# Optimization experiments

Hardware: AMD Instinct MI355X
Metric: run time of the kernel (lower is better)

## Reference

```python
import jax, jax.numpy as jnp
import numpy as np

D = 768      # qkv.in_features (ViT-Base)
R = 16       # LoRA rank
T = 8        # task_id: number of previously saved adapters
B_, S_ = 32, 256
TAU = 1.0


def setup_inputs() -> dict:
    key = jax.random.key(0)
    ks = jax.random.split(key, 13)
    s = lambda k, shape, sc=0.02: jax.random.normal(k, shape, jnp.float32) * sc
    return {
        "x": jax.random.normal(ks[0], (B_, S_, D), jnp.float32),
        "qkv_w": s(ks[1], (3 * D, D)),           # torch Linear weight [out,in]
        "qkv_b": s(ks[2], (3 * D,)),
        "la_q": s(ks[3], (R, D)),                # current-task LoRA A_q [r,d]
        "lb_q": s(ks[4], (D, R)),                # current-task LoRA B_q [d,r]
        "la_v": s(ks[5], (R, D)),
        "lb_v": s(ks[6], (D, R)),
        "A_q": s(ks[7], (T, R, D)),              # saved per-task A_q stacks
        "B_q": s(ks[8], (T, D, R)),
        "A_v": s(ks[9], (T, R, D)),
        "B_v": s(ks[10], (T, D, R)),
        "gate_logits": jax.random.normal(ks[11], (T,), jnp.float32),
        "alpha": jnp.ones((T + 1,), jnp.float32),  # gumbel_gate.alpha, indexed by task_id
    }


def _moe_branch(x, A, B, beta):
    """Weighted sum over T tasks of (x @ A_t^T @ B_t^T) / (||A_t||*||B_t||), weight beta_t.

    Vectorizes the per-task serial low-rank matmuls of the torch loop into two
    batched einsums; beta/norm scaling is folded into B to avoid materializing
    per-task [B,S,D] outputs.
    """
    nA = jnp.sqrt(jnp.sum(A * A, axis=(1, 2)))   # [T] Frobenius norms
    nB = jnp.sqrt(jnp.sum(B * B, axis=(1, 2)))
    scale = beta / (nA * nB)                      # [T]
    za = jnp.einsum('bsd,trd->bstr', x, A)       # [B,S,T,r]
    Bs = B * scale[:, None, None]                 # [T,D,r]
    return jnp.einsum('bstr,tdr->bsd', za, Bs)   # [B,S,D]


def _lora(x, a, b):
    # torch: b(a(x)) with Linear weights a:[r,d], b:[d,r]
    return jnp.einsum('bsr,dr->bsd', jnp.einsum('bsd,rd->bsr', x, a), b)


def reference(x, qkv_w, qkv_b, la_q, lb_q, la_v, lb_v, A_q, B_q, A_v, B_v, gate_logits, alpha):
    # Gumbel-softmax gate over tasks (deterministic/eval path: softmax(logits/tau), hard=False)
    beta = jax.nn.softmax(gate_logits / TAU)
    a_cur = alpha[T]  # alpha[self.task_id]
    new_q = _moe_branch(x, A_q, B_q, beta) + a_cur * _lora(x, la_q, lb_q)
    new_v = _moe_branch(x, A_v, B_v, beta) + a_cur * _lora(x, la_v, lb_v)
    qkv = jnp.einsum('bsd,ed->bse', x, qkv_w) + qkv_b  # [B,S,3D]
    qkv = qkv.at[..., :D].add(new_q)
    qkv = qkv.at[..., 2 * D:].add(new_v)
    return qkv
```

## Files before the change

### kernel.cpp

```cpp
#include <hip/hip_runtime.h>

#define TOK 8192
#define DD  768
#define NOUT 2304
#define TT  8
#define RR  16
#define KRANK 144

typedef __bf16 bf16;
typedef __bf16 bf16x4 __attribute__((ext_vector_type(4)));
typedef __bf16 bf16x8 __attribute__((ext_vector_type(8)));
typedef float  floatx4 __attribute__((ext_vector_type(4)));

__device__ __forceinline__ void gl_lds16(const void* g, void* l) {
    __builtin_amdgcn_global_load_lds((const __attribute__((address_space(1))) void*)g,
                                     (__attribute__((address_space(3))) void*)l, 16, 0, 0);
}

__global__ __launch_bounds__(256) void norms_kernel(
    const float* __restrict__ A_q, const float* __restrict__ B_q,
    const float* __restrict__ A_v, const float* __restrict__ B_v,
    float* __restrict__ norms)
{
    const int b = blockIdx.x;
    const float* base;
    switch (b >> 3) {
        case 0: base = A_q; break;
        case 1: base = B_q; break;
        case 2: base = A_v; break;
        default: base = B_v; break;
    }
    base += (b & 7) * (RR * DD);
    float s = 0.f;
    for (int i = threadIdx.x; i < RR * DD; i += 256) {
        float v = base[i];
        s = fmaf(v, v, s);
    }
    #pragma unroll
    for (int off = 32; off > 0; off >>= 1) s += __shfl_down(s, off);
    __shared__ float ws4[4];
    if ((threadIdx.x & 63) == 0) ws4[threadIdx.x >> 6] = s;
    __syncthreads();
    if (threadIdx.x == 0)
        norms[b] = sqrtf(ws4[0] + ws4[1] + ws4[2] + ws4[3]);
}

__global__ __launch_bounds__(64) void scales_kernel(
    const float* __restrict__ gate_logits, const float* __restrict__ alpha,
    const float* __restrict__ norms, float* __restrict__ scales)
{
    if (threadIdx.x == 0) {
        float mx = gate_logits[0];
        for (int t = 1; t < TT; ++t) mx = fmaxf(mx, gate_logits[t]);
        float e[TT], s = 0.f;
        for (int t = 0; t < TT; ++t) { e[t] = __expf(gate_logits[t] - mx); s += e[t]; }
        for (int t = 0; t < TT; ++t) {
            float beta = e[t] / s;
            scales[t]      = beta / (norms[t]      * norms[8 + t]);
            scales[8 + t]  = beta / (norms[16 + t] * norms[24 + t]);
        }
        scales[16] = alpha[TT];
    }
}

__global__ __launch_bounds__(256) void cast_x_kernel(
    const float* __restrict__ x, bf16* __restrict__ xb)
{
    const int idx = (blockIdx.x * 256 + threadIdx.x) * 4;
    const float4 v = *(const float4*)(x + idx);
    bf16x4 o = { (bf16)v.x, (bf16)v.y, (bf16)v.z, (bf16)v.w };
    *(bf16x4*)(xb + idx) = o;
}

__global__ __launch_bounds__(256) void cast_mid_kernel(
    const float* __restrict__ w, bf16* __restrict__ Wc)
{
    const int idx = DD * DD + (blockIdx.x * 256 + threadIdx.x) * 4;
    const float4 v = *(const float4*)(w + idx);
    bf16x4 o = { (bf16)v.x, (bf16)v.y, (bf16)v.z, (bf16)v.w };
    *(bf16x4*)(Wc + idx) = o;
}

__global__ __launch_bounds__(256) void fold_kernel(
    const float* __restrict__ qkv_w,
    const float* __restrict__ A_q, const float* __restrict__ la_q,
    const float* __restrict__ B_q, const float* __restrict__ lb_q,
    const float* __restrict__ A_v, const float* __restrict__ la_v,
    const float* __restrict__ B_v, const float* __restrict__ lb_v,
    const float* __restrict__ scales, bf16* __restrict__ Wc)
{
    __shared__ float c_lds[8 * KRANK];
    const int tid = threadIdx.x;
    const int d = blockIdx.x * 256 + tid;
    const int gy = blockIdx.y;
    const bool is_v = (gy >= 96);
    const int e0 = (is_v ? gy - 96 : gy) * 8;
    const float* Astack = is_v ? A_v : A_q;
    const float* la     = is_v ? la_v : la_q;
    const float* Bmat   = is_v ? B_v : B_q;
    const float* lb     = is_v ? lb_v : lb_q;
    const float* sc     = scales + (is_v ? 8 : 0);
    const float a_cur   = scales[16];
    const int rowbase   = (is_v ? 2 * DD : 0) + e0;

    for (int idx = tid; idx < 8 * KRANK; idx += 256) {
        const int j = idx / KRANK, i = idx - j * KRANK;
        const int e = e0 + j;
        float v;
        if (i < TT * RR) {
            const int t = i >> 4, r = i & 15;
            v = sc[t] * Bmat[(t * DD + e) * RR + r];
        } else {
            v = a_cur * lb[e * RR + (i - TT * RR)];
        }
        c_lds[j * KRANK + i] = v;
    }
    __syncthreads();

    float acc[8] = {0.f, 0.f, 0.f, 0.f, 0.f, 0.f, 0.f, 0.f};

    for (int i = 0; i < TT * RR; i += 4) {
        const float a0 = Astack[(i + 0) * DD + d];
        const float a1 = Astack[(i + 1) * DD + d];
        const float a2 = Astack[(i + 2) * DD + d];
        const float a3 = Astack[(i + 3) * DD + d];
        #pragma unroll
        for (int j = 0; j < 8; ++j) {
            const float4 cv = *(const float4*)&c_lds[j * KRANK + i];
            acc[j] = fmaf(a0, cv.x, fmaf(a1, cv.y, fmaf(a2, cv.z, fmaf(a3, cv.w, acc[j]))));
        }
    }
    #pragma unroll
    for (int i = 0; i < RR; i += 4) {
        const float a0 = la[(i + 0) * DD + d];
        const float a1 = la[(i + 1) * DD + d];
        const float a2 = la[(i + 2) * DD + d];
        const float a3 = la[(i + 3) * DD + d];
        #pragma unroll
        for (int j = 0; j < 8; ++j) {
            const float4 cv = *(const float4*)&c_lds[j * KRANK + TT * RR + i];
            acc[j] = fmaf(a0, cv.x, fmaf(a1, cv.y, fmaf(a2, cv.z, fmaf(a3, cv.w, acc[j]))));
        }
    }

    #pragma unroll
    for (int j = 0; j < 8; ++j) {
        const int row = rowbase + j;
        Wc[row * DD + d] = (bf16)(qkv_w[row * DD + d] + acc[j]);
    }
}

__global__ __launch_bounds__(256, 2) void gemm_kernel(
    const bf16* __restrict__ A, const bf16* __restrict__ B,
    const float* __restrict__ bias, float* __restrict__ C)
{
    __shared__ bf16 lds_a[128 * 64];
    __shared__ bf16 lds_b[128 * 64];
    const int tid  = threadIdx.x;
    const int lane = tid & 63;
    const int wave = tid >> 6;
    const int m0 = blockIdx.y * 128;
    const int n0 = blockIdx.x * 128;
    const int wm = (wave >> 1) * 64;
    const int wn = (wave & 1) * 64;

    const int srow = lane >> 3;
    const int scol = (lane & 7) * 8;

    floatx4 acc[4][4];
    #pragma unroll
    for (int i = 0; i < 4; ++i)
        #pragma unroll
        for (int j = 0; j < 4; ++j)
            acc[i][j] = (floatx4){0.f, 0.f, 0.f, 0.f};

    for (int kt = 0; kt < DD / 64; ++kt) {
        const int k0 = kt * 64;
        #pragma unroll
        for (int i = 0; i < 4; ++i) {
            const int j = i * 4 + wave;
            const int row = j * 8 + srow;
            gl_lds16(A + (m0 + row) * DD + k0 + scol, &lds_a[j * 512]);
            gl_lds16(B + (n0 + row) * DD + k0 + scol, &lds_b[j * 512]);
        }
        __syncthreads();
        #pragma unroll
        for (int ks = 0; ks < 2; ++ks) {
            bf16x8 af[4], bfr[4];
            const int kofs = ks * 32 + (lane >> 4) * 8;
            #pragma unroll
            for (int mt = 0; mt < 4; ++mt)
                af[mt] = *(const bf16x8*)&lds_a[(wm + mt * 16 + (lane & 15)) * 64 + kofs];
            #pragma unroll
            for (int nt = 0; nt < 4; ++nt)
                bfr[nt] = *(const bf16x8*)&lds_b[(wn + nt * 16 + (lane & 15)) * 64 + kofs];
            #pragma unroll
            for (int mt = 0; mt < 4; ++mt)
                #pragma unroll
                for (int nt = 0; nt < 4; ++nt)
                    acc[mt][nt] = __builtin_amdgcn_mfma_f32_16x16x32_bf16(
                        af[mt], bfr[nt], acc[mt][nt], 0, 0, 0);
        }
        __syncthreads();
    }

    const int cr = (lane >> 4) * 4;
    const int cc = lane & 15;
    #pragma unroll
    for (int nt = 0; nt < 4; ++nt) {
        const int gn = n0 + wn + nt * 16 + cc;
        const float bv = bias[gn];
        #pragma unroll
        for (int mt = 0; mt < 4; ++mt) {
            const int gmb = m0 + wm + mt * 16 + cr;
            #pragma unroll
            for (int r = 0; r < 4; ++r)
                C[(gmb + r) * NOUT + gn] = acc[mt][nt][r] + bv;
        }
    }
}

extern "C" void kernel_launch(void* const* d_in, const int* in_sizes, int n_in,
                              void* d_out, int out_size, void* d_ws, size_t ws_size,
                              hipStream_t stream)
{
    const float* x           = (const float*)d_in[0];
    const float* qkv_w       = (const float*)d_in[1];
    const float* qkv_b       = (const float*)d_in[2];
    const float* la_q        = (const float*)d_in[3];
    const float* lb_q        = (const float*)d_in[4];
    const float* la_v        = (const float*)d_in[5];
    const float* lb_v        = (const float*)d_in[6];
    const float* A_q         = (const float*)d_in[7];
    const float* B_q         = (const float*)d_in[8];
    const float* A_v         = (const float*)d_in[9];
    const float* B_v         = (const float*)d_in[10];
    const float* gate_logits = (const float*)d_in[11];
    const float* alpha       = (const float*)d_in[12];
    float* out = (float*)d_out;

    char* ws = (char*)d_ws;
    bf16*  Xbf    = (bf16*)ws;
    bf16*  Wc     = (bf16*)(ws + 12582912);
    float* norms  = (float*)(ws + 12582912 + 3538944);
    float* scales = norms + 32;

    norms_kernel <<<32, 256, 0, stream>>>(A_q, B_q, A_v, B_v, norms);
    scales_kernel<<<1, 64, 0, stream>>>(gate_logits, alpha, norms, scales);
    cast_x_kernel<<<TOK * DD / 1024, 256, 0, stream>>>(x, Xbf);
    cast_mid_kernel<<<DD * DD / 1024, 256, 0, stream>>>(qkv_w, Wc);
    fold_kernel  <<<dim3(3, 192), 256, 0, stream>>>(qkv_w,
                                                    A_q, la_q, B_q, lb_q,
                                                    A_v, la_v, B_v, lb_v,
                                                    scales, Wc);
    gemm_kernel  <<<dim3(NOUT / 128, TOK / 128), 256, 0, stream>>>(Xbf, Wc, qkv_b, out);
}
```

Before: 195.4 us.

## Merge prep kernels, XOR-swizzle LDS tiles, and remap GEMM blocks across XCDs

Six launches become three. The norm computation and the x bf16 cast now share one prep kernel. The softmax scale computation and the middle-weight cast move into the fold kernel, which each block computes redundantly. The GEMM now applies an XOR swizzle to LDS column chunks to cut bank conflicts on fragment reads, and remaps block indices so that blocks on the same XCD share M tiles for better L2 reuse. The goal is lower launch overhead and faster GEMM inner loops, at the cost of per-block softmax recomputation and mixed-role kernels.

```diff
diff --git a/kernel.cpp b/kernel.cpp
--- a/kernel.cpp
+++ b/kernel.cpp
@@ -17,68 +17,40 @@
                                      (__attribute__((address_space(3))) void*)l, 16, 0, 0);
 }
 
-__global__ __launch_bounds__(256) void norms_kernel(
+__global__ __launch_bounds__(256) void prep_kernel(
     const float* __restrict__ A_q, const float* __restrict__ B_q,
     const float* __restrict__ A_v, const float* __restrict__ B_v,
+    const float* __restrict__ x, bf16* __restrict__ xb,
     float* __restrict__ norms)
 {
+    __shared__ float ws4[4];
     const int b = blockIdx.x;
-    const float* base;
-    switch (b >> 3) {
-        case 0: base = A_q; break;
-        case 1: base = B_q; break;
-        case 2: base = A_v; break;
-        default: base = B_v; break;
-    }
-    base += (b & 7) * (RR * DD);
-    float s = 0.f;
-    for (int i = threadIdx.x; i < RR * DD; i += 256) {
-        float v = base[i];
-        s = fmaf(v, v, s);
-    }
-    #pragma unroll
-    for (int off = 32; off > 0; off >>= 1) s += __shfl_down(s, off);
-    __shared__ float ws4[4];
-    if ((threadIdx.x & 63) == 0) ws4[threadIdx.x >> 6] = s;
-    __syncthreads();
-    if (threadIdx.x == 0)
-        norms[b] = sqrtf(ws4[0] + ws4[1] + ws4[2] + ws4[3]);
-}
-
-__global__ __launch_bounds__(64) void scales_kernel(
-    const float* __restrict__ gate_logits, const float* __restrict__ alpha,
-    const float* __restrict__ norms, float* __restrict__ scales)
-{
-    if (threadIdx.x == 0) {
-        float mx = gate_logits[0];
-        for (int t = 1; t < TT; ++t) mx = fmaxf(mx, gate_logits[t]);
-        float e[TT], s = 0.f;
-        for (int t = 0; t < TT; ++t) { e[t] = __expf(gate_logits[t] - mx); s += e[t]; }
-        for (int t = 0; t < TT; ++t) {
-            float beta = e[t] / s;
-            scales[t]      = beta / (norms[t]      * norms[8 + t]);
-            scales[8 + t]  = beta / (norms[16 + t] * norms[24 + t]);
-        }
-        scales[16] = alpha[TT];
-    }
-}
-
-__global__ __launch_bounds__(256) void cast_x_kernel(
-    const float* __restrict__ x, bf16* __restrict__ xb)
-{
-    const int idx = (blockIdx.x * 256 + threadIdx.x) * 4;
-    const float4 v = *(const float4*)(x + idx);
-    bf16x4 o = { (bf16)v.x, (bf16)v.y, (bf16)v.z, (bf16)v.w };
-    *(bf16x4*)(xb + idx) = o;
-}
-
-__global__ __launch_bounds__(256) void cast_mid_kernel(
-    const float* __restrict__ w, bf16* __restrict__ Wc)
-{
-    const int idx = DD * DD + (blockIdx.x * 256 + threadIdx.x) * 4;
-    const float4 v = *(const float4*)(w + idx);
-    bf16x4 o = { (bf16)v.x, (bf16)v.y, (bf16)v.z, (bf16)v.w };
-    *(bf16x4*)(Wc + idx) = o;
+    if (b < 32) {
+        const float* base;
+        switch (b >> 3) {
+            case 0: base = A_q; break;
+            case 1: base = B_q; break;
+            case 2: base = A_v; break;
+            default: base = B_v; break;
+        }
+        base += (b & 7) * (RR * DD);
+        float s = 0.f;
+        for (int i = threadIdx.x; i < RR * DD; i += 256) {
+            float v = base[i];
+            s = fmaf(v, v, s);
+        }
+        #pragma unroll
+        for (int off = 32; off > 0; off >>= 1) s += __shfl_down(s, off);
+        if ((threadIdx.x & 63) == 0) ws4[threadIdx.x >> 6] = s;
+        __syncthreads();
+        if (threadIdx.x == 0)
+            norms[b] = sqrtf(ws4[0] + ws4[1] + ws4[2] + ws4[3]);
+    } else {
+        const int idx = ((b - 32) * 256 + threadIdx.x) * 4;
+        const float4 v = *(const float4*)(x + idx);
+        bf16x4 o = { (bf16)v.x, (bf16)v.y, (bf16)v.z, (bf16)v.w };
+        *(bf16x4*)(xb + idx) = o;
+    }
 }
 
 __global__ __launch_bounds__(256) void fold_kernel(
@@ -87,21 +59,46 @@
     const float* __restrict__ B_q, const float* __restrict__ lb_q,
     const float* __restrict__ A_v, const float* __restrict__ la_v,
     const float* __restrict__ B_v, const float* __restrict__ lb_v,
-    const float* __restrict__ scales, bf16* __restrict__ Wc)
-{
-    __shared__ float c_lds[8 * KRANK];
+    const float* __restrict__ gate_logits, const float* __restrict__ alpha,
+    const float* __restrict__ norms, bf16* __restrict__ Wc)
+{
     const int tid = threadIdx.x;
     const int d = blockIdx.x * 256 + tid;
     const int gy = blockIdx.y;
-    const bool is_v = (gy >= 96);
-    const int e0 = (is_v ? gy - 96 : gy) * 8;
+
+    if (gy >= 96 && gy < 192) {
+        const int rowbase = DD + (gy - 96) * 8;
+        #pragma unroll
+        for (int j = 0; j < 8; ++j) {
+            const int row = rowbase + j;
+            Wc[row * DD + d] = (bf16)qkv_w[row * DD + d];
+        }
+        return;
+    }
+
+    __shared__ float c_lds[8 * KRANK];
+    __shared__ float sc_sh[TT];
+    __shared__ float acur_sh;
+
+    const bool is_v = (gy >= 192);
+    const int e0 = (is_v ? gy - 192 : gy) * 8;
     const float* Astack = is_v ? A_v : A_q;
     const float* la     = is_v ? la_v : la_q;
     const float* Bmat   = is_v ? B_v : B_q;
     const float* lb     = is_v ? lb_v : lb_q;
-    const float* sc     = scales + (is_v ? 8 : 0);
-    const float a_cur   = scales[16];
+    const float* nA     = norms + (is_v ? 16 : 0);
+    const float* nB     = norms + (is_v ? 24 : 8);
     const int rowbase   = (is_v ? 2 * DD : 0) + e0;
+
+    if (tid == 0) {
+        float mx = gate_logits[0];
+        for (int t = 1; t < TT; ++t) mx = fmaxf(mx, gate_logits[t]);
+        float e[TT], s = 0.f;
+        for (int t = 0; t < TT; ++t) { e[t] = __expf(gate_logits[t] - mx); s += e[t]; }
+        for (int t = 0; t < TT; ++t) sc_sh[t] = (e[t] / s) / (nA[t] * nB[t]);
+        acur_sh = alpha[TT];
+    }
+    __syncthreads();
 
     for (int idx = tid; idx < 8 * KRANK; idx += 256) {
         const int j = idx / KRANK, i = idx - j * KRANK;
@@ -109,9 +106,9 @@
         float v;
         if (i < TT * RR) {
             const int t = i >> 4, r = i & 15;
-            v = sc[t] * Bmat[(t * DD + e) * RR + r];
+            v = sc_sh[t] * Bmat[(t * DD + e) * RR + r];
         } else {
-            v = a_cur * lb[e * RR + (i - TT * RR)];
+            v = acur_sh * lb[e * RR + (i - TT * RR)];
         }
         c_lds[j * KRANK + i] = v;
     }
@@ -159,13 +156,20 @@
     const int tid  = threadIdx.x;
     const int lane = tid & 63;
     const int wave = tid >> 6;
-    const int m0 = blockIdx.y * 128;
-    const int n0 = blockIdx.x * 128;
+
+    const int flat  = blockIdx.y * gridDim.x + blockIdx.x;
+    const int xcd   = flat & 7;
+    const int local = flat >> 3;
+    const int mb    = xcd * 8 + (local & 7);
+    const int nb    = local >> 3;
+    const int m0 = mb * 128;
+    const int n0 = nb * 128;
+
     const int wm = (wave >> 1) * 64;
     const int wn = (wave & 1) * 64;
 
     const int srow = lane >> 3;
-    const int scol = (lane & 7) * 8;
+    const int scol = ((lane & 7) ^ srow) * 8;
 
     floatx4 acc[4][4];
     #pragma unroll
@@ -187,13 +191,17 @@
         #pragma unroll
         for (int ks = 0; ks < 2; ++ks) {
             bf16x8 af[4], bfr[4];
-            const int kofs = ks * 32 + (lane >> 4) * 8;
-            #pragma unroll
-            for (int mt = 0; mt < 4; ++mt)
-                af[mt] = *(const bf16x8*)&lds_a[(wm + mt * 16 + (lane & 15)) * 64 + kofs];
-            #pragma unroll
-            for (int nt = 0; nt < 4; ++nt)
-                bfr[nt] = *(const bf16x8*)&lds_b[(wn + nt * 16 + (lane & 15)) * 64 + kofs];
+            const int c_log = ks * 4 + (lane >> 4);
+            #pragma unroll
+            for (int mt = 0; mt < 4; ++mt) {
+                const int r = wm + mt * 16 + (lane & 15);
+                af[mt] = *(const bf16x8*)&lds_a[r * 64 + ((c_log ^ (r & 7)) * 8)];
+            }
+            #pragma unroll
+            for (int nt = 0; nt < 4; ++nt) {
+                const int r = wn + nt * 16 + (lane & 15);
+                bfr[nt] = *(const bf16x8*)&lds_b[r * 64 + ((c_log ^ (r & 7)) * 8)];
+            }
             #pragma unroll
             for (int mt = 0; mt < 4; ++mt)
                 #pragma unroll
@@ -243,15 +251,12 @@
     bf16*  Xbf    = (bf16*)ws;
     bf16*  Wc     = (bf16*)(ws + 12582912);
     float* norms  = (float*)(ws + 12582912 + 3538944);
-    float* scales = norms + 32;
-
-    norms_kernel <<<32, 256, 0, stream>>>(A_q, B_q, A_v, B_v, norms);
-    scales_kernel<<<1, 64, 0, stream>>>(gate_logits, alpha, norms, scales);
-    cast_x_kernel<<<TOK * DD / 1024, 256, 0, stream>>>(x, Xbf);
-    cast_mid_kernel<<<DD * DD / 1024, 256, 0, stream>>>(qkv_w, Wc);
-    fold_kernel  <<<dim3(3, 192), 256, 0, stream>>>(qkv_w,
-                                                    A_q, la_q, B_q, lb_q,
-                                                    A_v, la_v, B_v, lb_v,
-                                                    scales, Wc);
-    gemm_kernel  <<<dim3(NOUT / 128, TOK / 128), 256, 0, stream>>>(Xbf, Wc, qkv_b, out);
-}
+
+    prep_kernel<<<32 + TOK * DD / 1024, 256, 0, stream>>>(A_q, B_q, A_v, B_v,
+                                                          x, Xbf, norms);
+    fold_kernel<<<dim3(3, 288), 256, 0, stream>>>(qkv_w,
+                                                  A_q, la_q, B_q, lb_q,
+                                                  A_v, la_v, B_v, lb_v,
+                                                  gate_logits, alpha, norms, Wc);
+    gemm_kernel<<<dim3(NOUT / 128, TOK / 128), 256, 0, stream>>>(Xbf, Wc, qkv_b, out);
+}
```

Result: faster. 174.6 us (-10.6%).
